# Optimization experiments

Hardware: AMD Instinct MI355X
Metric: run time of the kernel (lower is better)

## Reference

```python
import jax, jax.numpy as jnp
import numpy as np

BINS = 100
VMIN = 0.0
VMAX = 1.0
DELTA = (VMAX - VMIN) / BINS
EPS = 1e-5


def setup_inputs() -> dict:
    key = jax.random.key(0)
    x = jax.random.uniform(key, (32, 1048576), dtype=jnp.float32)  # [B, N] pixel values in [0,1]
    return {"x": x}


def reference(x):
    # bin centers: min + delta*(i + 0.5)
    centers = VMIN + DELTA * (jnp.arange(BINS, dtype=x.dtype) + 0.5)  # [bins]
    # Triangular-kernel soft count per bin: relu(delta - |x - c|) summed over N.
    # lax.map over the small fixed bin set keeps peak memory at one [B, N]
    # intermediate instead of materializing [bins, B, N].
    counts = jax.lax.map(
        lambda c: jnp.maximum(DELTA - jnp.abs(x - c), 0.0).sum(axis=1),
        centers,
    )  # [bins, B]
    out = counts.T  # [B, bins]
    # norm=True: divide each row by its sum (+eps)
    summ = out.sum(axis=1) + EPS  # [B]
    return out / summ[:, None]
```

## Files before the change

### kernel.cpp

```cpp
#include <hip/hip_runtime.h>


#define BINS 100
#define ROWS 101
#define BATCH 32
#define NPER 1048576
#define TPB 256
#define WAVES 4
#define COLS 32
#define BPR 24
#define GRID (BATCH * BPR)
#define NF4_ROW (NPER / 4)
#define HCELLS (WAVES * ROWS * COLS)

__device__ __forceinline__ int dppx1(int v) {
    return __builtin_amdgcn_update_dpp(v, v, 0xB1, 0xF, 0xF, false);
}

__global__ __launch_bounds__(TPB, 3) void hist_kernel(const float* __restrict__ x,
                                                      float* __restrict__ partial) {
    __shared__ uint32_t h[HCELLS];
    const int tid = threadIdx.x;

    uint4* h4 = reinterpret_cast<uint4*>(h);
    for (int i = tid; i < HCELLS / 4; i += TPB) h4[i] = make_uint4(0, 0, 0, 0);
    __syncthreads();

    const int row  = blockIdx.x / BPR;
    const int jblk = blockIdx.x % BPR;
    const int wave = tid >> 6;
    const int col  = (tid & 63) >> 1;
    uint32_t* hw = h + wave * (ROWS * COLS) + col;

    const float4* src = reinterpret_cast<const float4*>(x + (size_t)row * NPER);
    for (int i = jblk * TPB + tid; i < NF4_ROW; i += BPR * TPB) {
        float4 v = src[i];
#pragma unroll
        for (int p = 0; p < 2; ++p) {
            float a = p ? v.z : v.x;
            float b = p ? v.w : v.y;
            float Ua = __builtin_fmaf(a, 25600.0f, 128.0f);
            float Ub = __builtin_fmaf(b, 25600.0f, 128.0f);
            int ia = (int)Ua, ib = (int)Ub;
            int ra = ia >> 8, rb = ib >> 8;
            uint32_t inca = 0x10000u | (uint32_t)(ia & 255);
            uint32_t incb = 0x10000u | (uint32_t)(ib & 255);
            int pra = dppx1(ra), prb = dppx1(rb);
            uint32_t pia = (uint32_t)dppx1((int)inca);
            uint32_t pib = (uint32_t)dppx1((int)incb);
            uint32_t ta = inca, tb = incb;
            if (ra == rb)  { ta += incb; tb += inca; }
            if (ra == pra) ta += pia;
            if (ra == prb) ta += pib;
            if (rb == pra) tb += pia;
            if (rb == prb) tb += pib;
            uint32_t ca = hw[ra * COLS];
            uint32_t cb = hw[rb * COLS];
            hw[ra * COLS] = ca + ta;
            hw[rb * COLS] = cb + tb;
        }
    }
    __syncthreads();

    uint32_t s0 = 0, s1 = 0;
    const int a0 = tid, a1 = tid + TPB;
    {
        int w = a0 / ROWS, r = a0 - w * ROWS;
        const uint32_t* base = h + w * (ROWS * COLS) + r * COLS;
        uint32_t s = 0;
#pragma unroll
        for (int c = 0; c < COLS; ++c) s += base[(c + tid) & 31];
        s0 = s;
    }
    if (a1 < WAVES * ROWS) {
        int w = a1 / ROWS, r = a1 - w * ROWS;
        const uint32_t* base = h + w * (ROWS * COLS) + r * COLS;
        uint32_t s = 0;
#pragma unroll
        for (int c = 0; c < COLS; ++c) s += base[(c + tid) & 31];
        s1 = s;
    }
    __syncthreads();
    h[a0] = s0 >> 16;
    h[512 + a0] = s0 & 0xFFFFu;
    if (a1 < WAVES * ROWS) { h[a1] = s1 >> 16; h[512 + a1] = s1 & 0xFFFFu; }
    __syncthreads();
    if (tid < ROWS) {
        uint32_t N = h[tid] + h[101 + tid] + h[202 + tid] + h[303 + tid];
        uint32_t W = h[512 + tid] + h[613 + tid] + h[714 + tid] + h[815 + tid];
        h[1024 + tid] = N;
        h[1536 + tid] = W;
    }
    __syncthreads();
    if (tid < BINS) {
        float N1 = (float)h[1024 + tid + 1];
        float W1 = (float)h[1536 + tid + 1];
        float W0 = (float)h[1536 + tid];
        partial[blockIdx.x * BINS + tid] = N1 + (W0 - W1) * (1.0f / 256.0f);
    }
}

__global__ __launch_bounds__(128) void norm_kernel(const float* __restrict__ partial,
                                                   float* __restrict__ out) {
    __shared__ float sarr[2];
    const int row = blockIdx.x;
    const int t   = threadIdx.x;
    float cnt = 0.0f;
    if (t < BINS) {
        const float* p = partial + (size_t)row * BPR * BINS + t;
#pragma unroll
        for (int j = 0; j < BPR; ++j) cnt += p[j * BINS];
    }
    float s = cnt;
#pragma unroll
    for (int off = 32; off > 0; off >>= 1) s += __shfl_down(s, off);
    if ((t & 63) == 0) sarr[t >> 6] = s;
    __syncthreads();
    const float total = sarr[0] + sarr[1];
    if (t < BINS) {
        out[row * BINS + t] = 0.01f * cnt / (0.01f * total + 1e-5f);
    }
}

extern "C" void kernel_launch(void* const* d_in, const int* in_sizes, int n_in,
                              void* d_out, int out_size, void* d_ws, size_t ws_size,
                              hipStream_t stream) {
    const float* x = (const float*)d_in[0];
    float* out = (float*)d_out;
    float* partial = (float*)d_ws;

    hist_kernel<<<GRID, TPB, 0, stream>>>(x, partial);
    norm_kernel<<<BATCH, 128, 0, stream>>>(partial, out);
}
```

Measured before the change: 34.40 us.

## Share histogram columns across 4 lanes with quad DPP merging, halve LDS

Each histogram column is now shared by four lanes instead of two, and the four lanes in a quad merge their increments with three DPP exchanges before one lane-private read-modify-write. This halves the LDS histogram, so the launch bound is raised to 6 blocks per CU and blocks per row doubled to 48. Each element is handled independently rather than in pairs. The aim is higher occupancy to hide global load latency, at the cost of more DPP/compare work per element and more partial rows for the normalization kernel to reduce.

```diff
diff --git a/kernel.cpp b/kernel.cpp
--- a/kernel.cpp
+++ b/kernel.cpp
@@ -7,17 +7,19 @@
 #define NPER 1048576
 #define TPB 256
 #define WAVES 4
-#define COLS 32
-#define BPR 24
+#define COLS 16
+#define BPR 48
 #define GRID (BATCH * BPR)
 #define NF4_ROW (NPER / 4)
+#define STRIDE (BPR * TPB)
 #define HCELLS (WAVES * ROWS * COLS)
 
-__device__ __forceinline__ int dppx1(int v) {
-    return __builtin_amdgcn_update_dpp(v, v, 0xB1, 0xF, 0xF, false);
+template <int PAT>
+__device__ __forceinline__ int dpp(int v) {
+    return __builtin_amdgcn_update_dpp(v, v, PAT, 0xF, 0xF, false);
 }
 
-__global__ __launch_bounds__(TPB, 3) void hist_kernel(const float* __restrict__ x,
+__global__ __launch_bounds__(TPB, 6) void hist_kernel(const float* __restrict__ x,
                                                       float* __restrict__ partial) {
     __shared__ uint32_t h[HCELLS];
     const int tid = threadIdx.x;
@@ -29,35 +31,28 @@
     const int row  = blockIdx.x / BPR;
     const int jblk = blockIdx.x % BPR;
     const int wave = tid >> 6;
-    const int col  = (tid & 63) >> 1;
+    const int col  = (tid & 63) >> 2;
     uint32_t* hw = h + wave * (ROWS * COLS) + col;
 
     const float4* src = reinterpret_cast<const float4*>(x + (size_t)row * NPER);
-    for (int i = jblk * TPB + tid; i < NF4_ROW; i += BPR * TPB) {
+    for (int i = jblk * TPB + tid; i < NF4_ROW; i += STRIDE) {
         float4 v = src[i];
+        float vv[4] = {v.x, v.y, v.z, v.w};
 #pragma unroll
-        for (int p = 0; p < 2; ++p) {
-            float a = p ? v.z : v.x;
-            float b = p ? v.w : v.y;
-            float Ua = __builtin_fmaf(a, 25600.0f, 128.0f);
-            float Ub = __builtin_fmaf(b, 25600.0f, 128.0f);
-            int ia = (int)Ua, ib = (int)Ub;
-            int ra = ia >> 8, rb = ib >> 8;
-            uint32_t inca = 0x10000u | (uint32_t)(ia & 255);
-            uint32_t incb = 0x10000u | (uint32_t)(ib & 255);
-            int pra = dppx1(ra), prb = dppx1(rb);
-            uint32_t pia = (uint32_t)dppx1((int)inca);
-            uint32_t pib = (uint32_t)dppx1((int)incb);
-            uint32_t ta = inca, tb = incb;
-            if (ra == rb)  { ta += incb; tb += inca; }
-            if (ra == pra) ta += pia;
-            if (ra == prb) ta += pib;
-            if (rb == pra) tb += pia;
-            if (rb == prb) tb += pib;
-            uint32_t ca = hw[ra * COLS];
-            uint32_t cb = hw[rb * COLS];
-            hw[ra * COLS] = ca + ta;
-            hw[rb * COLS] = cb + tb;
+        for (int e = 0; e < 4; ++e) {
+            float U = __builtin_fmaf(vv[e], 25600.0f, 128.0f);
+            int  iU = (int)U;
+            int   r = iU >> 8;
+            uint32_t inc = 0x10000u | (uint32_t)(iU & 255);
+            int r1 = dpp<0xB1>(r);  uint32_t i1 = (uint32_t)dpp<0xB1>((int)inc);
+            int r2 = dpp<0x4E>(r);  uint32_t i2 = (uint32_t)dpp<0x4E>((int)inc);
+            int r3 = dpp<0x1B>(r);  uint32_t i3 = (uint32_t)dpp<0x1B>((int)inc);
+            uint32_t tot = inc;
+            if (r == r1) tot += i1;
+            if (r == r2) tot += i2;
+            if (r == r3) tot += i3;
+            uint32_t c = hw[r * COLS];
+            hw[r * COLS] = c + tot;
         }
     }
     __syncthreads();
@@ -69,7 +64,7 @@
         const uint32_t* base = h + w * (ROWS * COLS) + r * COLS;
         uint32_t s = 0;
 #pragma unroll
-        for (int c = 0; c < COLS; ++c) s += base[(c + tid) & 31];
+        for (int c = 0; c < COLS; ++c) s += base[(c + tid) & (COLS - 1)];
         s0 = s;
     }
     if (a1 < WAVES * ROWS) {
@@ -77,7 +72,7 @@
         const uint32_t* base = h + w * (ROWS * COLS) + r * COLS;
         uint32_t s = 0;
 #pragma unroll
-        for (int c = 0; c < COLS; ++c) s += base[(c + tid) & 31];
+        for (int c = 0; c < COLS; ++c) s += base[(c + tid) & (COLS - 1)];
         s1 = s;
     }
     __syncthreads();
```

Result: slower. 35.60 us (+3.5%).
